# Kernel optimization log

Hardware: AMD Instinct MI355X
Metric: run time of the kernel (lower is better)

Reference implementation:

```python
import jax, jax.numpy as jnp
import numpy as np

V_REST = 0.0
V_RESET = 0.0
V_TH = 1.27
TAU = 50.0
SPIKE_DURATION = 1
SCALE = 100.0  # SurrGradSpike.scale


@jax.custom_vjp
def spike(x):
    return (x > 0).astype(x.dtype)

def _spike_fwd(x):
    return (x > 0).astype(x.dtype), x

def _spike_bwd(x, g):
    # normalized negative part of fast sigmoid (Zenke & Ganguli 2018)
    return (g / (SCALE * jnp.abs(x) + 1.0) ** 2,)

spike.defvjp(_spike_fwd, _spike_bwd)


def _shift(a, k):
    # a[:, j] -> a[:, j + k], zero padded out of range
    if k == 0:
        return a
    if k > 0:
        return jnp.pad(a[:, k:], ((0, 0), (0, k)))
    return jnp.pad(a[:, :k], ((0, 0), (-k, 0)))


def _lif(ode, decay):
    ode2 = ode[..., 0]          # [B, T]
    B, T = ode2.shape
    ode_t = ode2.T              # [T, B] for scan

    def step(carry, inp):
        v, counter, z = carry   # z = remaining steps whose dv reads are zeroed
        t, x = inp
        v = v - decay * (v - V_REST)
        v = jnp.where(counter == 1, V_RESET, v)
        # dv[:, t] was zeroed by a spike within the previous 5 steps (torch in-place window)
        x_eff = jnp.where(z > 0, 0.0, x)
        v = v + x_eff
        v = jnp.where(counter > 1, V_TH, v)
        s = spike(v - V_TH)
        s_d = jax.lax.stop_gradient(s)
        counter = counter + (SPIKE_DURATION + 1) * s_d
        v = jnp.where(counter > 1, V_TH, v)
        # spike at t zeroes dv[:, t-1:t+6]; at t==0 the torch slice [-1:6] is empty
        z = jnp.where((s_d > 0) & (t >= 1), 5.0, jnp.maximum(z - 1.0, 0.0))
        counter = jnp.maximum(counter - 1.0, 0.0)
        return (v, counter, z), (v, s, s_d)

    v0 = jnp.full((B,), V_REST, dtype=ode2.dtype)
    c0 = jnp.zeros((B,), dtype=ode2.dtype)
    z0 = jnp.zeros((B,), dtype=ode2.dtype)
    ts = jnp.arange(T)
    _, (v_rec, s_rec, sd_rec) = jax.lax.scan(step, (v0, c0, z0), (ts, ode_t))
    v_rec = v_rec.T             # [B, T]
    s_rec = s_rec.T             # [B, T]

    sp = sd_rec.T > 0           # detached spike mask [B, T]
    sp = sp.at[:, 0].set(False)  # spike at t=0 zeroes nothing (empty slice in torch)
    # column j of dv is zeroed iff a spike occurred at t' in [j-5, j+1]
    zero_mask = jnp.zeros_like(sp)
    for k in range(-5, 2):
        zero_mask = zero_mask | _shift(sp, k)
    dv = jnp.where(zero_mask, 0.0, ode2)
    return v_rec, s_rec, dv


def setup_inputs() -> dict:
    key = jax.random.key(0)
    B, T = 2048, 4096
    ode = jax.random.normal(key, (B, T, 1), dtype=jnp.float32)
    decay = jnp.float32(1.0 / TAU)  # LIF.decay parameter (learn_tau=False)
    return {"ode": ode, "decay": decay}


def reference(ode, decay):
    return _lif(ode, decay)
```

## Files before the change

### kernel.cpp

```cpp
#include <hip/hip_runtime.h>

constexpr int   T   = 4096;
constexpr float VTH = 1.27f;
constexpr int   K   = 32;
constexpr int   L   = T / K;
constexpr int   LG  = L / 4;
constexpr int   WGG = 160;

__device__ __forceinline__ bool sstep(float x, float decay, float& v, unsigned& h, bool& gate) {
    float t1 = __fmul_rn(decay, v);
    float vd = __fsub_rn(v, t1);
    float xe = gate ? 0.0f : x;
    float vn = __fadd_rn(vd, xe);
    bool  s  = vn > VTH;
    v = s ? 0.0f : vn;
    bool g4 = (h & 15u) != 0u;
    h = (h << 1) | (s ? 1u : 0u);
    gate = s || g4;
    return s;
}

__device__ __forceinline__ bool ostep(float x, float decay, float& v, unsigned& h, bool& gate,
                                      float& vo, float& so, float& dvo, float xprev) {
    float t1 = __fmul_rn(decay, v);
    float vd = __fsub_rn(v, t1);
    float xe = gate ? 0.0f : x;
    float vn = __fadd_rn(vd, xe);
    bool  s  = vn > VTH;
    vo = s ? VTH  : vn;
    so = s ? 1.0f : 0.0f;
    v  = s ? 0.0f : vn;
    bool z6 = s || ((h & 63u) != 0u);
    dvo = z6 ? 0.0f : xprev;
    bool g4 = (h & 15u) != 0u;
    h = (h << 1) | (s ? 1u : 0u);
    gate = s || g4;
    return s;
}

__device__ __forceinline__ void ogroup(float4 X, float decay, float& v, unsigned& h, bool& gate,
                                       float& xprev, float4& vo, float4& so,
                                       float& close, float& px, float& py, float& pz) {
    ostep(X.x, decay, v, h, gate, vo.x, so.x, close, xprev); xprev = X.x;
    ostep(X.y, decay, v, h, gate, vo.y, so.y, px,    xprev); xprev = X.y;
    ostep(X.z, decay, v, h, gate, vo.z, so.z, py,    xprev); xprev = X.z;
    ostep(X.w, decay, v, h, gate, vo.w, so.w, pz,    xprev); xprev = X.w;
}

#define WVM(N) do { asm volatile("s_waitcnt vmcnt(" #N ")" ::: "memory"); \
                    __builtin_amdgcn_sched_barrier(0); } while (0)
#define WLG()  do { asm volatile("s_waitcnt lgkmcnt(0)" ::: "memory"); \
                    __builtin_amdgcn_sched_barrier(0); } while (0)

using GU32 = const __attribute__((address_space(1))) unsigned int;
using LU32 = __attribute__((address_space(3))) unsigned int;

__device__ __forceinline__ void stage8(const float* src0, float4* lbuf) {
    LU32* lp = (LU32*)lbuf;
#pragma unroll
    for (int j = 0; j < 8; ++j)
        __builtin_amdgcn_global_load_lds((GU32*)(src0 + (size_t)j * 8 * T),
                                         lp + j * 256, 16, 0, 0);
}

__device__ __forceinline__ void flush_pair(int p, int tid, int rb, int k,
        float* __restrict__ vout, float* __restrict__ sout, float* __restrict__ dvout,
        const float4 (*tv)[8], const float4 (*ts)[8], const float4 (*td)[64][8]) {
    WLG();
    const int cc = (tid & 7) ^ (tid >> 3);
#pragma unroll
    for (int jj = 0; jj < 8; ++jj) {
        int rr = jj * 8 + (tid >> 3);
        size_t off = (size_t)(rb + rr) * T + k * L + p * 32 + (tid & 7) * 4;
        *(float4*)(vout + off) = tv[rr][cc];
        *(float4*)(sout + off) = ts[rr][cc];
        if (p >= 1) *(float4*)(dvout + off - 32) = td[(p - 1) & 1][rr][cc];
    }
    WLG();
}

__global__ __launch_bounds__(64, 1)
void lif_spec(const float* __restrict__ ode, const float* __restrict__ decay_p,
              float* __restrict__ vout, float* __restrict__ sout, float* __restrict__ dvout,
              float2* __restrict__ Sst, float2* __restrict__ Est, int B) {
    __shared__ float4 xin[64 * 8];
    __shared__ float4 tv[64][8];
    __shared__ float4 ts[64][8];
    __shared__ float4 td[2][64][8];

    const int tid = threadIdx.x;
    const int gg  = blockIdx.x * 64;
    const int rb  = gg % B;
    const int k   = gg / B;
    const int b   = rb + tid;
    const float decay = decay_p[0];
    const int xs7 = tid & 7;

    const int g0f = k * LG;
    const int wgg = (k == 0) ? 0 : (g0f < WGG ? g0f : WGG);
    const int nw  = wgg >> 3;
    const int gstart = g0f - wgg;

    float v = 0.0f; unsigned h = 0u; bool gate = false;
    float xprev = 0.0f;

    float xla = (k < K - 1) ? ode[(size_t)b * T + (size_t)(k + 1) * L] : 0.0f;

#define STAGE(t) stage8(ode + ((size_t)(rb + (tid >> 3)) * T \
                               + (size_t)(gstart + 8 * (t)) * 4 + (tid & 7) * 4), xin)
#define RD8 const float4* xr = xin + (size_t)tid * 8; \
            float4 G0 = xr[0], G1 = xr[1], G2 = xr[2], G3 = xr[3], \
                   G4 = xr[4], G5 = xr[5], G6 = xr[6], G7 = xr[7];
#define WG4(G) { sstep(G.x, decay, v, h, gate); sstep(G.y, decay, v, h, gate); \
                 sstep(G.z, decay, v, h, gate); sstep(G.w, decay, v, h, gate); }

    STAGE(0);

    if (nw > 0) {
        const bool t0row = (gstart == 0);
        for (int t = 0; t < nw; ++t) {
            WVM(0);
            RD8
            WLG();
            STAGE(t + 1);
            if (t == 0 && t0row) {
                sstep(G0.x, decay, v, h, gate); h = 0u; gate = false;
                sstep(G0.y, decay, v, h, gate);
                sstep(G0.z, decay, v, h, gate);
                sstep(G0.w, decay, v, h, gate);
            } else { WG4(G0) }
            WG4(G1) WG4(G2) WG4(G3) WG4(G4) WG4(G5) WG4(G6) WG4(G7)
        }
    }

    float4 Pd;

#define OG(X, gidx) { float4 V_, S_; float cl_, p0_, p1_, p2_; \
        ogroup(X, decay, v, h, gate, xprev, V_, S_, cl_, p0_, p1_, p2_); \
        if ((gidx) > 0) { Pd.w = cl_; \
            td[(((gidx) - 1) >> 3) & 1][tid][(((gidx) - 1) & 7) ^ xs7] = Pd; } \
        Pd.x = p0_; Pd.y = p1_; Pd.z = p2_; \
        tv[tid][((gidx) & 7) ^ xs7] = V_; ts[tid][((gidx) & 7) ^ xs7] = S_; }

    {
        WVM(0);
        RD8
        WLG();
        STAGE(nw + 1);
        if (nw > 0) Sst[k * B + b] = make_float2(v, __uint_as_float(h & 127u));
        if (k == 0) {
            float4 V_, S_; float dvd;
            bool s0 = ostep(G0.x, decay, v, h, gate, V_.x, S_.x, dvd, xprev); xprev = G0.x;
            h = 0u; gate = false;
            bool s1 = ostep(G0.y, decay, v, h, gate, V_.y, S_.y, Pd.x, xprev); xprev = G0.y;
            ostep(G0.z, decay, v, h, gate, V_.z, S_.z, Pd.y, xprev); xprev = G0.z;
            ostep(G0.w, decay, v, h, gate, V_.w, S_.w, Pd.z, xprev); xprev = G0.w;
            if (s0 && s1) V_.z = VTH;
            tv[tid][xs7] = V_; ts[tid][xs7] = S_;
        } else {
            float4 V_, S_; float cl_;
            ogroup(G0, decay, v, h, gate, xprev, V_, S_, cl_, Pd.x, Pd.y, Pd.z);
            tv[tid][xs7] = V_; ts[tid][xs7] = S_;
        }
        OG(G1, 1) OG(G2, 2) OG(G3, 3) OG(G4, 4) OG(G5, 5) OG(G6, 6) OG(G7, 7)
        flush_pair(0, tid, rb, k, vout, sout, dvout, tv, ts, td);
    }
    {
        WVM(16);
        RD8
        WLG();
        STAGE(nw + 2);
        OG(G0, 8)  OG(G1, 9)  OG(G2, 10) OG(G3, 11)
        OG(G4, 12) OG(G5, 13) OG(G6, 14) OG(G7, 15)
        flush_pair(1, tid, rb, k, vout, sout, dvout, tv, ts, td);
    }
    {
        WVM(24);
        RD8
        WLG();
        STAGE(nw + 3);
        OG(G0, 16) OG(G1, 17) OG(G2, 18) OG(G3, 19)
        OG(G4, 20) OG(G5, 21) OG(G6, 22) OG(G7, 23)
        flush_pair(2, tid, rb, k, vout, sout, dvout, tv, ts, td);
    }
    {
        WVM(24);
        RD8
        OG(G0, 24) OG(G1, 25) OG(G2, 26) OG(G3, 27)
        OG(G4, 28) OG(G5, 29) OG(G6, 30) OG(G7, 31)
        flush_pair(3, tid, rb, k, vout, sout, dvout, tv, ts, td);
    }
#undef OG
#undef RD8
#undef WG4
#undef STAGE

    Est[k * B + b] = make_float2(v, __uint_as_float(h & 127u));

    if (k < K - 1) {
        float vo_, so_;
        ostep(xla, decay, v, h, gate, vo_, so_, Pd.w, xprev);
    } else {
        Pd.w = ((h & 63u) != 0u) ? 0.0f : xprev;
    }
    td[1][tid][7 ^ xs7] = Pd;
    WLG();
    {
        const int cc = (tid & 7) ^ (tid >> 3);
#pragma unroll
        for (int jj = 0; jj < 8; ++jj) {
            int rr = jj * 8 + (tid >> 3);
            size_t off = (size_t)(rb + rr) * T + k * L + 3 * 32 + (tid & 7) * 4;
            *(float4*)(dvout + off) = td[1][rr][cc];
        }
    }
}

__global__ __launch_bounds__(64, 1)
void lif_fix(const float* __restrict__ ode, const float* __restrict__ decay_p,
             float* __restrict__ vout, float* __restrict__ sout, float* __restrict__ dvout,
             const float2* __restrict__ Sst, const float2* __restrict__ Est, int B) {
    const int b = blockIdx.x * 64 + threadIdx.x;
    const float decay = decay_p[0];

    float2 E  = Est[b];
    float2 S1 = Sst[B + b];
    float2 E1 = Est[B + b];
    for (int k = 1; k < K; ++k) {
        float2 S = S1, Ek = E1;
        if (k + 1 < K) { S1 = Sst[(k + 1) * B + b]; E1 = Est[(k + 1) * B + b]; }
        bool match = (S.x == E.x) && (__float_as_uint(S.y) == __float_as_uint(E.y));
        if (match) { E = Ek; continue; }

        const size_t bt = (size_t)b * T;
        const float4* __restrict__ x4 = (const float4*)(ode + bt);
        float4* __restrict__ v4 = (float4*)(vout + bt);
        float4* __restrict__ s4 = (float4*)(sout + bt);
        float4* __restrict__ d4 = (float4*)(dvout + bt);
        const int g0f = k * LG;

        float v = E.x; unsigned h = __float_as_uint(E.y);
        bool gate = (h & 31u) != 0u;
        float xprev = 0.0f;
        float4 pend;

        float4 Q0 = x4[g0f], Q1 = x4[g0f + 1], Q2 = x4[g0f + 2], Q3 = x4[g0f + 3];
        {
            float4 vo, so; float cl;
            ogroup(Q0, decay, v, h, gate, xprev, vo, so, cl, pend.x, pend.y, pend.z);
            v4[g0f] = vo; s4[g0f] = so;
            Q0 = x4[g0f + 4];
        }
#define FPROC(cc, Q) { float4 vo, so; float px, py, pz; \
            ogroup(Q, decay, v, h, gate, xprev, vo, so, pend.w, px, py, pz); \
            d4[g0f + (cc) - 1] = pend; \
            pend.x = px; pend.y = py; pend.z = pz; \
            v4[g0f + (cc)] = vo; s4[g0f + (cc)] = so; }
        FPROC(1, Q1) Q1 = x4[g0f + 5];
        FPROC(2, Q2) Q2 = x4[g0f + 6];
        FPROC(3, Q3) Q3 = x4[g0f + 7];
        for (int c0 = 4; c0 < LG; c0 += 4) {
            FPROC(c0,     Q0) Q0 = x4[g0f + (c0 + 4 < LG ? c0 + 4 : LG - 1)];
            FPROC(c0 + 1, Q1) Q1 = x4[g0f + (c0 + 5 < LG ? c0 + 5 : LG - 1)];
            FPROC(c0 + 2, Q2) Q2 = x4[g0f + (c0 + 6 < LG ? c0 + 6 : LG - 1)];
            FPROC(c0 + 3, Q3) Q3 = x4[g0f + (c0 + 7 < LG ? c0 + 7 : LG - 1)];
        }
#undef FPROC
        E = make_float2(v, __uint_as_float(h & 127u));
        if (k < K - 1) {
            float xla = ode[bt + (size_t)(k + 1) * L];
            float vo_, so_;
            ostep(xla, decay, v, h, gate, vo_, so_, pend.w, xprev);
        } else {
            pend.w = ((h & 63u) != 0u) ? 0.0f : xprev;
        }
        d4[g0f + LG - 1] = pend;
    }
}

extern "C" void kernel_launch(void* const* d_in, const int* in_sizes, int n_in,
                              void* d_out, int out_size, void* d_ws, size_t ws_size,
                              hipStream_t stream) {
    const float* ode   = (const float*)d_in[0];
    const float* decay = (const float*)d_in[1];
    float* out = (float*)d_out;

    const int BT = in_sizes[0];
    const int B  = BT / T;

    float* vout  = out;
    float* sout  = out + (size_t)BT;
    float* dvout = out + 2 * (size_t)BT;

    float2* Sst = (float2*)d_ws;
    float2* Est = Sst + (size_t)K * B;

    lif_spec<<<dim3((B * K) / 64), dim3(64), 0, stream>>>(ode, decay, vout, sout, dvout,
                                                          Sst, Est, B);
    lif_fix<<<dim3(B / 64), dim3(64), 0, stream>>>(ode, decay, vout, sout, dvout,
                                                   Sst, Est, B);
}
```

Before: 171.4 us.

## Double time chunks to 64, keep outputs in registers, and swizzle staged loads

Splits the time axis into 64 chunks instead of 32, so each workgroup handles 64 steps (two 32-step halves) and twice as many workgroups run, giving more parallel speculative work. Per-step v, s and dv results now stay in registers and are written out through a single small swizzled LDS staging buffer, replacing the larger tv/ts/td shared arrays. Global-to-LDS staging is XOR-swizzled to avoid bank conflicts, and launch bounds allow two workgroups per CU. The cost is a warmup replay that is a larger share of each shorter chunk, more chunk boundaries for the fix-up pass to check, and higher register pressure.

```diff
diff --git a/kernel.cpp b/kernel.cpp
--- a/kernel.cpp
+++ b/kernel.cpp
@@ -2,7 +2,7 @@
 
 constexpr int   T   = 4096;
 constexpr float VTH = 1.27f;
-constexpr int   K   = 32;
+constexpr int   K   = 64;
 constexpr int   L   = T / K;
 constexpr int   LG  = L / 4;
 constexpr int   WGG = 160;
@@ -63,30 +63,12 @@
                                          lp + j * 256, 16, 0, 0);
 }
 
-__device__ __forceinline__ void flush_pair(int p, int tid, int rb, int k,
-        float* __restrict__ vout, float* __restrict__ sout, float* __restrict__ dvout,
-        const float4 (*tv)[8], const float4 (*ts)[8], const float4 (*td)[64][8]) {
-    WLG();
-    const int cc = (tid & 7) ^ (tid >> 3);
-#pragma unroll
-    for (int jj = 0; jj < 8; ++jj) {
-        int rr = jj * 8 + (tid >> 3);
-        size_t off = (size_t)(rb + rr) * T + k * L + p * 32 + (tid & 7) * 4;
-        *(float4*)(vout + off) = tv[rr][cc];
-        *(float4*)(sout + off) = ts[rr][cc];
-        if (p >= 1) *(float4*)(dvout + off - 32) = td[(p - 1) & 1][rr][cc];
-    }
-    WLG();
-}
-
-__global__ __launch_bounds__(64, 1)
+__global__ __launch_bounds__(64, 2)
 void lif_spec(const float* __restrict__ ode, const float* __restrict__ decay_p,
               float* __restrict__ vout, float* __restrict__ sout, float* __restrict__ dvout,
               float2* __restrict__ Sst, float2* __restrict__ Est, int B) {
     __shared__ float4 xin[64 * 8];
-    __shared__ float4 tv[64][8];
-    __shared__ float4 ts[64][8];
-    __shared__ float4 td[2][64][8];
+    __shared__ float4 stg[64 * 8];
 
     const int tid = threadIdx.x;
     const int gg  = blockIdx.x * 64;
@@ -94,7 +76,8 @@
     const int k   = gg / B;
     const int b   = rb + tid;
     const float decay = decay_p[0];
-    const int xs7 = tid & 7;
+    const int t7 = tid & 7, t3 = tid >> 3;
+    const int sw = t7 ^ t3;
 
     const int g0f = k * LG;
     const int wgg = (k == 0) ? 0 : (g0f < WGG ? g0f : WGG);
@@ -106,11 +89,13 @@
 
     float xla = (k < K - 1) ? ode[(size_t)b * T + (size_t)(k + 1) * L] : 0.0f;
 
-#define STAGE(t) stage8(ode + ((size_t)(rb + (tid >> 3)) * T \
-                               + (size_t)(gstart + 8 * (t)) * 4 + (tid & 7) * 4), xin)
-#define RD8 const float4* xr = xin + (size_t)tid * 8; \
-            float4 G0 = xr[0], G1 = xr[1], G2 = xr[2], G3 = xr[3], \
-                   G4 = xr[4], G5 = xr[5], G6 = xr[6], G7 = xr[7];
+#define STAGE(t) stage8(ode + ((size_t)(rb + t3) * T \
+                               + (size_t)(gstart + 8 * (t)) * 4 + sw * 4), xin)
+    float4 G0, G1, G2, G3, G4, G5, G6, G7;
+#define RD8() do { G0 = xin[tid*8 + (0^t7)]; G1 = xin[tid*8 + (1^t7)]; \
+                   G2 = xin[tid*8 + (2^t7)]; G3 = xin[tid*8 + (3^t7)]; \
+                   G4 = xin[tid*8 + (4^t7)]; G5 = xin[tid*8 + (5^t7)]; \
+                   G6 = xin[tid*8 + (6^t7)]; G7 = xin[tid*8 + (7^t7)]; } while (0)
 #define WG4(G) { sstep(G.x, decay, v, h, gate); sstep(G.y, decay, v, h, gate); \
                  sstep(G.z, decay, v, h, gate); sstep(G.w, decay, v, h, gate); }
 
@@ -120,7 +105,7 @@
         const bool t0row = (gstart == 0);
         for (int t = 0; t < nw; ++t) {
             WVM(0);
-            RD8
+            RD8();
             WLG();
             STAGE(t + 1);
             if (t == 0 && t0row) {
@@ -133,87 +118,84 @@
         }
     }
 
-    float4 Pd;
-
-#define OG(X, gidx) { float4 V_, S_; float cl_, p0_, p1_, p2_; \
-        ogroup(X, decay, v, h, gate, xprev, V_, S_, cl_, p0_, p1_, p2_); \
-        if ((gidx) > 0) { Pd.w = cl_; \
-            td[(((gidx) - 1) >> 3) & 1][tid][(((gidx) - 1) & 7) ^ xs7] = Pd; } \
-        Pd.x = p0_; Pd.y = p1_; Pd.z = p2_; \
-        tv[tid][((gidx) & 7) ^ xs7] = V_; ts[tid][((gidx) & 7) ^ xs7] = S_; }
+    float4 VA0, VA1, VA2, VA3, VA4, VA5, VA6, VA7;
+    float4 SA0, SA1, SA2, SA3, SA4, SA5, SA6, SA7;
+    float4 DA0, DA1, DA2, DA3, DA4, DA5, DA6, DA7;
+    float4 DB0, DB1, DB2, DB3, DB4, DB5, DB6, DB7;
+    float dumm;
+
+#define OGR(X, Vd, Sd, CloseL, Dd) { \
+        ostep(X.x, decay, v, h, gate, Vd.x, Sd.x, CloseL, xprev); xprev = X.x; \
+        ostep(X.y, decay, v, h, gate, Vd.y, Sd.y, Dd.x,   xprev); xprev = X.y; \
+        ostep(X.z, decay, v, h, gate, Vd.z, Sd.z, Dd.y,   xprev); xprev = X.z; \
+        ostep(X.w, decay, v, h, gate, Vd.w, Sd.w, Dd.z,   xprev); xprev = X.w; }
+
+#define FL(R0,R1,R2,R3,R4,R5,R6,R7, dst, poff) { \
+        stg[tid*8 + (0^t7)] = R0; stg[tid*8 + (1^t7)] = R1; \
+        stg[tid*8 + (2^t7)] = R2; stg[tid*8 + (3^t7)] = R3; \
+        stg[tid*8 + (4^t7)] = R4; stg[tid*8 + (5^t7)] = R5; \
+        stg[tid*8 + (6^t7)] = R6; stg[tid*8 + (7^t7)] = R7; \
+        WLG(); \
+        _Pragma("unroll") \
+        for (int jj = 0; jj < 8; ++jj) { \
+            int rr = jj * 8 + t3; \
+            size_t off = (size_t)(rb + rr) * T + (size_t)k * L + (poff) * 32 + t7 * 4; \
+            *(float4*)((dst) + off) = stg[rr * 8 + sw]; \
+        } \
+        WLG(); }
 
     {
         WVM(0);
-        RD8
+        RD8();
         WLG();
+        if (nw > 0) Sst[k * B + b] = make_float2(v, __uint_as_float(h & 127u));
         STAGE(nw + 1);
-        if (nw > 0) Sst[k * B + b] = make_float2(v, __uint_as_float(h & 127u));
         if (k == 0) {
-            float4 V_, S_; float dvd;
-            bool s0 = ostep(G0.x, decay, v, h, gate, V_.x, S_.x, dvd, xprev); xprev = G0.x;
+            bool s0 = ostep(G0.x, decay, v, h, gate, VA0.x, SA0.x, dumm, xprev); xprev = G0.x;
             h = 0u; gate = false;
-            bool s1 = ostep(G0.y, decay, v, h, gate, V_.y, S_.y, Pd.x, xprev); xprev = G0.y;
-            ostep(G0.z, decay, v, h, gate, V_.z, S_.z, Pd.y, xprev); xprev = G0.z;
-            ostep(G0.w, decay, v, h, gate, V_.w, S_.w, Pd.z, xprev); xprev = G0.w;
-            if (s0 && s1) V_.z = VTH;
-            tv[tid][xs7] = V_; ts[tid][xs7] = S_;
+            bool s1 = ostep(G0.y, decay, v, h, gate, VA0.y, SA0.y, DA0.x, xprev); xprev = G0.y;
+            ostep(G0.z, decay, v, h, gate, VA0.z, SA0.z, DA0.y, xprev); xprev = G0.z;
+            ostep(G0.w, decay, v, h, gate, VA0.w, SA0.w, DA0.z, xprev); xprev = G0.w;
+            if (s0 && s1) VA0.z = VTH;
         } else {
-            float4 V_, S_; float cl_;
-            ogroup(G0, decay, v, h, gate, xprev, V_, S_, cl_, Pd.x, Pd.y, Pd.z);
-            tv[tid][xs7] = V_; ts[tid][xs7] = S_;
-        }
-        OG(G1, 1) OG(G2, 2) OG(G3, 3) OG(G4, 4) OG(G5, 5) OG(G6, 6) OG(G7, 7)
-        flush_pair(0, tid, rb, k, vout, sout, dvout, tv, ts, td);
-    }
+            OGR(G0, VA0, SA0, dumm, DA0)
+        }
+        OGR(G1, VA1, SA1, DA0.w, DA1) OGR(G2, VA2, SA2, DA1.w, DA2)
+        OGR(G3, VA3, SA3, DA2.w, DA3) OGR(G4, VA4, SA4, DA3.w, DA4)
+        OGR(G5, VA5, SA5, DA4.w, DA5) OGR(G6, VA6, SA6, DA5.w, DA6)
+        OGR(G7, VA7, SA7, DA6.w, DA7)
+        FL(VA0, VA1, VA2, VA3, VA4, VA5, VA6, VA7, vout, 0)
+        FL(SA0, SA1, SA2, SA3, SA4, SA5, SA6, SA7, sout, 0)
+    }
+
     {
         WVM(16);
-        RD8
+        RD8();
         WLG();
-        STAGE(nw + 2);
-        OG(G0, 8)  OG(G1, 9)  OG(G2, 10) OG(G3, 11)
-        OG(G4, 12) OG(G5, 13) OG(G6, 14) OG(G7, 15)
-        flush_pair(1, tid, rb, k, vout, sout, dvout, tv, ts, td);
-    }
-    {
-        WVM(24);
-        RD8
-        WLG();
-        STAGE(nw + 3);
-        OG(G0, 16) OG(G1, 17) OG(G2, 18) OG(G3, 19)
-        OG(G4, 20) OG(G5, 21) OG(G6, 22) OG(G7, 23)
-        flush_pair(2, tid, rb, k, vout, sout, dvout, tv, ts, td);
-    }
-    {
-        WVM(24);
-        RD8
-        OG(G0, 24) OG(G1, 25) OG(G2, 26) OG(G3, 27)
-        OG(G4, 28) OG(G5, 29) OG(G6, 30) OG(G7, 31)
-        flush_pair(3, tid, rb, k, vout, sout, dvout, tv, ts, td);
-    }
-#undef OG
+        OGR(G0, VA0, SA0, DA7.w, DB0)
+        FL(DA0, DA1, DA2, DA3, DA4, DA5, DA6, DA7, dvout, 0)
+        OGR(G1, VA1, SA1, DB0.w, DB1) OGR(G2, VA2, SA2, DB1.w, DB2)
+        OGR(G3, VA3, SA3, DB2.w, DB3) OGR(G4, VA4, SA4, DB3.w, DB4)
+        OGR(G5, VA5, SA5, DB4.w, DB5) OGR(G6, VA6, SA6, DB5.w, DB6)
+        OGR(G7, VA7, SA7, DB6.w, DB7)
+        FL(VA0, VA1, VA2, VA3, VA4, VA5, VA6, VA7, vout, 1)
+        FL(SA0, SA1, SA2, SA3, SA4, SA5, SA6, SA7, sout, 1)
+    }
+
+    Est[k * B + b] = make_float2(v, __uint_as_float(h & 127u));
+
+    if (k < K - 1) {
+        float vo_, so_;
+        ostep(xla, decay, v, h, gate, vo_, so_, DB7.w, xprev);
+    } else {
+        DB7.w = ((h & 63u) != 0u) ? 0.0f : xprev;
+    }
+    FL(DB0, DB1, DB2, DB3, DB4, DB5, DB6, DB7, dvout, 1)
+#undef OGR
+#undef FL
 #undef RD8
 #undef WG4
 #undef STAGE
-
-    Est[k * B + b] = make_float2(v, __uint_as_float(h & 127u));
-
-    if (k < K - 1) {
-        float vo_, so_;
-        ostep(xla, decay, v, h, gate, vo_, so_, Pd.w, xprev);
-    } else {
-        Pd.w = ((h & 63u) != 0u) ? 0.0f : xprev;
-    }
-    td[1][tid][7 ^ xs7] = Pd;
-    WLG();
-    {
-        const int cc = (tid & 7) ^ (tid >> 3);
-#pragma unroll
-        for (int jj = 0; jj < 8; ++jj) {
-            int rr = jj * 8 + (tid >> 3);
-            size_t off = (size_t)(rb + rr) * T + k * L + 3 * 32 + (tid & 7) * 4;
-            *(float4*)(dvout + off) = td[1][rr][cc];
-        }
-    }
 }
 
 __global__ __launch_bounds__(64, 1)
```

After: 191.6 us. 11.8% more time.
